# Kernel optimization log

Measured on AMD Instinct MI355X. Metric: run time of the kernel, lower is better.

The kernel has to match this reference:

```python
import jax, jax.numpy as jnp
import numpy as np

K = 4
N_UP = 50
N_DOWN = 50


def setup_inputs() -> dict:
    key = jax.random.key(0)
    k1, k2, k3, k4 = jax.random.split(key, 4)
    B, N, D = 2048, 100, 128
    configs = jax.random.randint(k1, (B, N), 0, 4, dtype=jnp.int64)
    tok_table = jax.random.normal(k2, (4, D), dtype=jnp.float32)
    pos_table = jax.random.normal(k3, (144, D), dtype=jnp.float32)
    W_orb = jax.random.normal(k4, (K * (N_UP + N_DOWN), D), dtype=jnp.float32) * 0.01
    b_orb = jnp.zeros((K * (N_UP + N_DOWN),), dtype=jnp.float32)
    return {"configs": configs, "tok_table": tok_table, "pos_table": pos_table,
            "W_orb": W_orb, "b_orb": b_orb}


def _occ_idx(mask, n_occ):
    # indices of occupied sites first (stable argsort of -mask), then sorted ascending
    idx = jnp.argsort(-mask.astype(jnp.float32), axis=1)[:, :n_occ]
    return jnp.sort(idx, axis=1)


def reference(configs, tok_table, pos_table, W_orb, b_orb):
    B, N = configs.shape
    # encode_input + identity backbone
    h = tok_table[configs] + pos_table[jnp.arange(N)][None, :, :]  # (B,N,D)
    orb = jnp.einsum('bnd,od->bno', h, W_orb) + b_orb               # (B,N,K*(nu+nd))
    orb_up = orb[..., :K * N_UP].reshape(B, N, K, N_UP).transpose(0, 2, 1, 3)
    orb_dn = orb[..., K * N_UP:].reshape(B, N, K, N_DOWN).transpose(0, 2, 1, 3)
    has_up = (configs == 1) | (configs == 3)
    has_dn = (configs == 2) | (configs == 3)
    up_idx = _occ_idx(has_up, N_UP)      # (B,n_up)
    dn_idx = _occ_idx(has_dn, N_DOWN)    # (B,n_down)
    phi_up = jnp.take_along_axis(orb_up, up_idx[:, None, :, None], axis=2)  # (B,K,nu,nu)
    phi_dn = jnp.take_along_axis(orb_dn, dn_idx[:, None, :, None], axis=2)  # (B,K,nd,nd)
    det_up = jnp.linalg.det(phi_up)  # (B,K)
    det_dn = jnp.linalg.det(phi_dn)  # (B,K)
    psi = jnp.sum(det_up * det_dn, axis=1)  # (B,)
    log_abs = jnp.log(jnp.abs(psi) + 1e-30)
    phase = jnp.where(psi >= 0, 0.0, jnp.pi).astype(jnp.float32)
    return jax.lax.complex(log_abs.astype(jnp.float32), phase)
```

## Files before the change

### kernel.cpp

```cpp
#include <hip/hip_runtime.h>
#include <math.h>

#define NSITE 100
#define NOCC  50
#define DIM   128
#define KDET  4
#define NTAB  400
#define TP_FLOATS ((4 + 144) * NTAB)


__device__ __forceinline__ unsigned dpp_max64_to_lane63(unsigned x) {
  unsigned t;
  t = (unsigned)__builtin_amdgcn_update_dpp((int)x, (int)x, 0x111, 0xf, 0xf, false);
  x = x > t ? x : t;
  t = (unsigned)__builtin_amdgcn_update_dpp((int)x, (int)x, 0x112, 0xf, 0xf, false);
  x = x > t ? x : t;
  t = (unsigned)__builtin_amdgcn_update_dpp((int)x, (int)x, 0x114, 0xf, 0xf, false);
  x = x > t ? x : t;
  t = (unsigned)__builtin_amdgcn_update_dpp((int)x, (int)x, 0x118, 0xf, 0xf, false);
  x = x > t ? x : t;
  t = (unsigned)__builtin_amdgcn_update_dpp((int)x, (int)x, 0x142, 0xa, 0xf, false);
  x = x > t ? x : t;
  t = (unsigned)__builtin_amdgcn_update_dpp((int)x, (int)x, 0x143, 0xc, 0xf, false);
  x = x > t ? x : t;
  return x;
}

#define REPB(X) X(0) X(1) X(2) X(3) X(4) X(5) X(6) X(7) X(8) X(9) \
  X(10) X(11) X(12) X(13) X(14) X(15) X(16) X(17) X(18) X(19) \
  X(20) X(21) X(22) X(23) X(24) X(25) X(26) X(27) X(28) X(29) \
  X(30) X(31) X(32) X(33) X(34) X(35) X(36) X(37) X(38) X(39) \
  X(40) X(41) X(42) X(43) X(44) X(45) X(46) X(47) X(48) X(49)

#define LUPAIR(X) \
  X(0,1) X(1,2) X(2,3) X(3,4) X(4,5) X(5,6) X(6,7) X(7,8) X(8,9) X(9,10) \
  X(10,11) X(11,12) X(12,13) X(13,14) X(14,15) X(15,16) X(16,17) X(17,18) \
  X(18,19) X(19,20) X(20,21) X(21,22) X(22,23) X(23,24) X(24,25) X(25,26) \
  X(26,27) X(27,28) X(28,29) X(29,30) X(30,31) X(31,32) X(32,33) X(33,34) \
  X(34,35) X(35,36) X(36,37) X(37,38) X(38,39) X(39,40) X(40,41) X(41,42) \
  X(42,43) X(43,44) X(44,45) X(45,46) X(46,47) X(47,48) X(48,49)

__global__ __launch_bounds__(256) void tp_kernel(
    const float* __restrict__ tok, const float* __restrict__ pos,
    const float* __restrict__ W,   const float* __restrict__ bvec,
    float* __restrict__ T, float* __restrict__ P)
{
  const int gid = blockIdx.x * 256 + threadIdx.x;
  if (gid >= 148 * NTAB) return;
  const int row = gid / NTAB;
  const int col = gid - row * NTAB;
  const float4* h4 = (const float4*)((row < 4) ? (tok + (size_t)row * DIM)
                                               : (pos + (size_t)(row - 4) * DIM));
  const float4* w4 = (const float4*)(W + (size_t)col * DIM);
  float acc = 0.0f;
  #pragma unroll
  for (int i = 0; i < DIM / 4; ++i) {
    float4 a = h4[i], b = w4[i];
    acc = fmaf(a.x, b.x, acc);
    acc = fmaf(a.y, b.y, acc);
    acc = fmaf(a.z, b.z, acc);
    acc = fmaf(a.w, b.w, acc);
  }
  if (row < 4) T[(size_t)row * NTAB + col] = acc;
  else         P[(size_t)(row - 4) * NTAB + col] = acc + bvec[col];
}

__global__ __launch_bounds__(256)
__attribute__((amdgpu_waves_per_eu(6)))
void det_kernel(
    const int*   __restrict__ configs,
    const float* __restrict__ T,
    const float* __restrict__ P,
    double*      __restrict__ dets)
{
  const int b    = blockIdx.x;
  const int spin = blockIdx.y;

  __shared__ int cfg[NSITE];
  __shared__ int idx[NOCC];
  __shared__ unsigned long long omask[2];

  const int tid = threadIdx.x;

  bool occv = false;
  if (tid < NSITE) {
    const int c = configs[(size_t)b * NSITE + tid];
    cfg[tid] = c;
    occv = (spin == 0) ? (c == 1 || c == 3) : (c == 2 || c == 3);
  }
  const unsigned long long bal = __ballot(occv);
  if ((tid & 63) == 0 && tid < 128) omask[tid >> 6] = bal;
  __syncthreads();
  if (tid < NSITE) {
    const unsigned long long m0 = omask[0], m1 = omask[1];
    const int mtot = __popcll(m0) + __popcll(m1);
    const int need = (mtot < NOCC) ? (NOCC - mtot) : 0;
    int pocc;
    if (tid >= 64) pocc = __popcll(m0) + __popcll(m1 & ((1ull << (tid - 64)) - 1ull));
    else           pocc = __popcll(m0 & ((1ull << tid) - 1ull));
    const int punocc = tid - pocc;
    const bool sel = occv ? (pocc < NOCC) : (punocc < need);
    const int  poscap = (pocc  < NOCC) ? pocc  : NOCC;
    const int  pfill  = (punocc < need) ? punocc : need;
    if (sel) idx[poscap + pfill] = tid;
  }
  __syncthreads();

  const int lane = tid & 63;
  const int wave = tid >> 6;
  const int wave_u  = __builtin_amdgcn_readfirstlane(wave);
  const int colbase = spin * 200 + wave_u * 50;

  const bool act  = (lane < NOCC);
  const int  site = idx[act ? lane : 0];
  const int  cc0  = cfg[site];
  const float2* T2 = (const float2*)(T + (size_t)cc0  * NTAB + colbase);
  const float2* P2 = (const float2*)(P + (size_t)site * NTAB + colbase);

  #define DECLQ(i) float q##i;
  REPB(DECLQ)
  #undef DECLQ
  #define LQ(i0, i1) { float2 a = T2[(i0) / 2], c = P2[(i0) / 2]; \
      q##i0 = a.x + c.x; q##i1 = a.y + c.y; }
  LQ(0, 1)  LQ(2, 3)  LQ(4, 5)  LQ(6, 7)  LQ(8, 9)  LQ(10, 11)
  __builtin_amdgcn_sched_barrier(0);
  LQ(12, 13) LQ(14, 15) LQ(16, 17) LQ(18, 19) LQ(20, 21) LQ(22, 23)
  __builtin_amdgcn_sched_barrier(0);
  LQ(24, 25) LQ(26, 27) LQ(28, 29) LQ(30, 31) LQ(32, 33) LQ(34, 35)
  __builtin_amdgcn_sched_barrier(0);
  LQ(36, 37) LQ(38, 39) LQ(40, 41) LQ(42, 43) LQ(44, 45) LQ(46, 47)
  __builtin_amdgcn_sched_barrier(0);
  LQ(48, 49)
  #undef LQ

  #define ZEROQ(i) q##i = act ? q##i : 0.0f;
  REPB(ZEROQ)
  #undef ZEROQ

  __builtin_amdgcn_sched_barrier(0);

  unsigned aliveq = act ? 0xFFFFFFFFu : 0u;
  float    mant_prod = 1.0f;
  int      esum = 0;
  unsigned sgnx = 0u;
  unsigned long long chosen = 0ull;
  int      invsum = 0;
  const unsigned lu = (unsigned)lane;

  unsigned keyv;
  int   p;
  float rp;

  #define PIVFIN(Jx) { \
    p = __builtin_amdgcn_readlane((int)keyv, 63) & 63; \
    const float piv = __int_as_float( \
        __builtin_amdgcn_readlane(__float_as_int(q##Jx), p)); \
    const unsigned pb = __float_as_uint(piv); \
    esum += (int)((pb >> 23) & 0xFFu) - 127; \
    sgnx ^= (pb & 0x80000000u); \
    mant_prod *= __uint_as_float((pb & 0x007FFFFFu) | 0x3F800000u); \
    invsum += __popcll(chosen >> (p + 1)); \
    chosen |= 1ull << (unsigned)p; \
    aliveq = ((unsigned)lane == (unsigned)p) ? 0u : aliveq; \
    float r0 = __builtin_amdgcn_rcpf(piv); \
    r0 = fmaf(fmaf(-piv, r0, 1.0f), r0, r0); \
    rp = ((pb & 0x7FFFFFFFu) != 0u) ? r0 : 0.0f; }

  #define UPDC(CC) if ((CC) > cJ1) { \
      const float pc = __int_as_float( \
          __builtin_amdgcn_readlane(__float_as_int(q##CC), p)); \
      q##CC = fmaf(-mult, pc, q##CC); }

  #define LUS(J, J1) { \
    const float mult = __uint_as_float(__float_as_uint(q##J * rp) & aliveq); \
    { const float pc0 = __int_as_float( \
          __builtin_amdgcn_readlane(__float_as_int(q##J1), p)); \
      q##J1 = fmaf(-mult, pc0, q##J1); } \
    keyv = ((__float_as_uint(q##J1) & 0x7FFFFFC0u) | lu) & aliveq; \
    keyv = dpp_max64_to_lane63(keyv); \
    const int cJ1 = (J1); \
    REPB(UPDC) \
    PIVFIN(J1) \
  }

  keyv = ((__float_as_uint(q0) & 0x7FFFFFC0u) | lu) & aliveq;
  keyv = dpp_max64_to_lane63(keyv);
  PIVFIN(0)
  LUPAIR(LUS)
  #undef LUS
  #undef UPDC
  #undef PIVFIN

  const double logdet =
      log((double)mant_prod) + (double)esum * 0.6931471805599453;
  const int sgn = (((sgnx >> 31) + (unsigned)invsum) & 1u) ? -1 : 1;

  if (lane == 0) {
    size_t o = (((size_t)b * 2 + spin) * KDET + wave) * 2;
    dets[o]     = logdet;
    dets[o + 1] = (double)sgn;
  }
}

__global__ __launch_bounds__(256) void combine_kernel(
    const double* __restrict__ dets, float* __restrict__ out, int B)
{
  int b = blockIdx.x * blockDim.x + threadIdx.x;
  if (b >= B) return;
  const double* du = dets + ((size_t)b * 2 + 0) * KDET * 2;
  const double* dd = dets + ((size_t)b * 2 + 1) * KDET * 2;
  double t[KDET], s[KDET], m = -1e300;
  #pragma unroll
  for (int k = 0; k < KDET; ++k) {
    t[k] = du[2 * k] + dd[2 * k];
    s[k] = du[2 * k + 1] * dd[2 * k + 1];
    if (t[k] > m) m = t[k];
  }
  double sum = 0.0;
  #pragma unroll
  for (int k = 0; k < KDET; ++k) {
    if (t[k] > -1e290) sum += s[k] * exp(t[k] - m);
  }
  double p  = (m > -1e290) ? exp(m) * fabs(sum) : 0.0;
  double la = log(p + 1e-30);
  float phase = (sum >= 0.0) ? 0.0f : 3.14159265358979f;
  out[b]     = (float)la;
  out[B + b] = phase;
}

extern "C" void kernel_launch(void* const* d_in, const int* in_sizes, int n_in,
                              void* d_out, int out_size, void* d_ws, size_t ws_size,
                              hipStream_t stream) {
  const int*   configs = (const int*)  d_in[0];
  const float* tok     = (const float*)d_in[1];
  const float* pos     = (const float*)d_in[2];
  const float* W       = (const float*)d_in[3];
  const float* bv      = (const float*)d_in[4];

  float*  wsf  = (float*)d_ws;
  float*  T    = wsf;
  float*  P    = wsf + 4 * NTAB;
  double* dets = (double*)(wsf + TP_FLOATS);
  const int B = in_sizes[0] / NSITE;

  tp_kernel<<<(148 * NTAB + 255) / 256, 256, 0, stream>>>(tok, pos, W, bv, T, P);
  dim3 grid(B, 2);
  det_kernel<<<grid, 256, 0, stream>>>(configs, T, P, dets);
  combine_kernel<<<(B + 255) / 256, 256, 0, stream>>>(dets, (float*)d_out, B);
}
```

Before: 226.4 us.

## Replace fully unrolled LU elimination with a rolled loop using register shifting

The 49 fully unrolled elimination steps, each with a triangular set of column updates, become a single non-unrolled loop body. Each iteration updates all remaining columns and shifts them down one register slot, so the current pivot column always sits in q0. This shrinks instruction footprint and instruction-cache pressure. The cost is that every step now processes all 49 columns, including already-eliminated zeros, so the arithmetic roughly doubles.

```diff
diff --git a/kernel.cpp b/kernel.cpp
--- a/kernel.cpp
+++ b/kernel.cpp
@@ -32,8 +32,8 @@
   X(30) X(31) X(32) X(33) X(34) X(35) X(36) X(37) X(38) X(39) \
   X(40) X(41) X(42) X(43) X(44) X(45) X(46) X(47) X(48) X(49)
 
-#define LUPAIR(X) \
-  X(0,1) X(1,2) X(2,3) X(3,4) X(4,5) X(5,6) X(6,7) X(7,8) X(8,9) X(9,10) \
+#define REPU(X) \
+  X(1,2) X(2,3) X(3,4) X(4,5) X(5,6) X(6,7) X(7,8) X(8,9) X(9,10) \
   X(10,11) X(11,12) X(12,13) X(13,14) X(14,15) X(15,16) X(16,17) X(17,18) \
   X(18,19) X(19,20) X(20,21) X(21,22) X(22,23) X(23,24) X(24,25) X(25,26) \
   X(26,27) X(27,28) X(28,29) X(29,30) X(30,31) X(31,32) X(32,33) X(33,34) \
@@ -151,45 +151,41 @@
   int   p;
   float rp;
 
-  #define PIVFIN(Jx) { \
+  #define PIVFIN0 { \
     p = __builtin_amdgcn_readlane((int)keyv, 63) & 63; \
-    const float piv = __int_as_float( \
-        __builtin_amdgcn_readlane(__float_as_int(q##Jx), p)); \
-    const unsigned pb = __float_as_uint(piv); \
+    const unsigned pb = (unsigned)__builtin_amdgcn_readlane( \
+        __float_as_int(q0), p); \
     esum += (int)((pb >> 23) & 0xFFu) - 127; \
     sgnx ^= (pb & 0x80000000u); \
     mant_prod *= __uint_as_float((pb & 0x007FFFFFu) | 0x3F800000u); \
     invsum += __popcll(chosen >> (p + 1)); \
     chosen |= 1ull << (unsigned)p; \
     aliveq = ((unsigned)lane == (unsigned)p) ? 0u : aliveq; \
+    const float piv = __uint_as_float(pb); \
     float r0 = __builtin_amdgcn_rcpf(piv); \
     r0 = fmaf(fmaf(-piv, r0, 1.0f), r0, r0); \
     rp = ((pb & 0x7FFFFFFFu) != 0u) ? r0 : 0.0f; }
 
-  #define UPDC(CC) if ((CC) > cJ1) { \
-      const float pc = __int_as_float( \
-          __builtin_amdgcn_readlane(__float_as_int(q##CC), p)); \
-      q##CC = fmaf(-mult, pc, q##CC); }
-
-  #define LUS(J, J1) { \
-    const float mult = __uint_as_float(__float_as_uint(q##J * rp) & aliveq); \
-    { const float pc0 = __int_as_float( \
-          __builtin_amdgcn_readlane(__float_as_int(q##J1), p)); \
-      q##J1 = fmaf(-mult, pc0, q##J1); } \
-    keyv = ((__float_as_uint(q##J1) & 0x7FFFFFC0u) | lu) & aliveq; \
-    keyv = dpp_max64_to_lane63(keyv); \
-    const int cJ1 = (J1); \
-    REPB(UPDC) \
-    PIVFIN(J1) \
-  }
-
   keyv = ((__float_as_uint(q0) & 0x7FFFFFC0u) | lu) & aliveq;
   keyv = dpp_max64_to_lane63(keyv);
-  PIVFIN(0)
-  LUPAIR(LUS)
-  #undef LUS
-  #undef UPDC
-  #undef PIVFIN
+  PIVFIN0
+
+  #define USH(L, L1) { const float pc = __int_as_float( \
+      __builtin_amdgcn_readlane(__float_as_int(q##L1), p)); \
+      q##L = fmaf(-mult, pc, q##L1); }
+
+  #pragma unroll 1
+  for (int J = 0; J < 49; ++J) {
+    const float mult = __uint_as_float(__float_as_uint(q0 * rp) & aliveq);
+    USH(0, 1)
+    keyv = ((__float_as_uint(q0) & 0x7FFFFFC0u) | lu) & aliveq;
+    keyv = dpp_max64_to_lane63(keyv);
+    REPU(USH)
+    q49 = 0.0f;
+    PIVFIN0
+  }
+  #undef USH
+  #undef PIVFIN0
 
   const double logdet =
       log((double)mant_prod) + (double)esum * 0.6931471805599453;
```

After: 316.6 us. +39.8%, slower.
